# Kernel tuning notes

Hardware: AMD Instinct MI355X
Metric: run time of the kernel (lower is better)

## Reference

```python
import jax, jax.numpy as jnp
import numpy as np

N, C, D = 2048, 1000, 768
KNN = 5          # module default
SIGMA = 1.0      # unused by kNN affinity (matches original kNN_affinity)
BOUND_LAMBDA = 1.0
MAX_STEPS = 100


def setup_inputs() -> dict:
    key = jax.random.key(0)
    k1, k2 = jax.random.split(key)
    logits = jax.random.normal(k1, (N, C), dtype=jnp.float32) * 2.0
    feats = jax.random.normal(k2, (N, D), dtype=jnp.float32)
    return {"logits": logits, "feats": feats}


def _knn_affinity(feats, knn):
    # feats are L2-normalized, so squared euclidean dist = 2 - 2 * <xi, xj>
    n = feats.shape[0]
    sim = feats @ feats.T                                  # [N, N]
    dist = jnp.sqrt(jnp.clip(2.0 - 2.0 * sim, 0.0))        # [N, N]
    _, idx = jax.lax.top_k(-dist, knn + 1)                 # knn+1 smallest distances
    idx = idx[:, 1:]                                       # drop self (dist 0)
    W = jnp.zeros((n, n), dtype=feats.dtype)
    W = W.at[jnp.arange(n)[:, None], idx].set(1.0)
    return W


def _entropy_energy(Y, unary, pairwise, lam):
    return jnp.sum(unary * Y - lam * pairwise * Y + Y * jnp.log(jnp.clip(Y, 1e-20)))


def _laplacian_optimization(unary, kernel, lam=BOUND_LAMBDA, max_steps=MAX_STEPS):
    Y0 = jax.nn.softmax(-unary, axis=-1)

    def cond(state):
        _, _, i, done = state
        return (i < max_steps) & jnp.logical_not(done)

    def body(state):
        Y, oldE, i, _ = state
        pairwise = lam * (kernel @ Y)                      # [N, C]
        Ynew = jax.nn.softmax(pairwise - unary, axis=-1)
        E = _entropy_energy(Ynew, unary, pairwise, lam)
        done = (i > 1) & (jnp.abs(E - oldE) <= 1e-8 * jnp.abs(oldE))
        return (Ynew, E, i + 1, done)

    Y, _, _, _ = jax.lax.while_loop(
        cond, body, (Y0, jnp.float32(jnp.inf), jnp.int32(0), jnp.array(False))
    )
    return Y


def reference(logits, feats):
    probas = jax.nn.softmax(logits, axis=1)
    unary = -jnp.log(probas + 1e-10)                       # [N, C]
    f = feats / jnp.linalg.norm(feats, axis=-1, keepdims=True)
    kernel = _knn_affinity(f, KNN)                         # [N, N] binary
    kernel = 0.5 * (kernel + kernel.T)                     # force_symmetry=True
    return _laplacian_optimization(unary, kernel)
```

## Files before the change

kernel.cpp:

```cpp
#include <hip/hip_runtime.h>
#include <hip/hip_cooperative_groups.h>
#include <math.h>

namespace cg = cooperative_groups;

#define N_ 2048
#define C_ 1000
#define D_ 768
#define K_ 5
#define CAP_ 128
#define MAXS_ 100
#define LB_ 128
#define LT_ 512

typedef unsigned short ushort_t;
typedef unsigned int uint_t;

__device__ inline float bflo(uint_t v) { union { uint_t i; float f; } c; c.i = v << 16; return c.f; }
__device__ inline float bfhi(uint_t v) { union { uint_t i; float f; } c; c.i = v & 0xffff0000u; return c.f; }
__device__ inline ushort_t f2b(float f) {
    union { float f; uint_t i; } c; c.f = f;
    return (ushort_t)((c.i + 0x7fffu + ((c.i >> 16) & 1u)) >> 16);
}
__device__ inline uint_t pk(float a, float b) { return (uint_t)f2b(a) | ((uint_t)f2b(b) << 16); }

__global__ __launch_bounds__(256) void k_norm(const float* __restrict__ feats,
                                              float* __restrict__ fn) {
    const int r = blockIdx.x, tid = threadIdx.x;
    __shared__ float red[256];
    const float* row = feats + (size_t)r * D_;
    float ss = 0.f;
    for (int c = tid; c < D_; c += 256) { float v = row[c]; ss += v * v; }
    red[tid] = ss; __syncthreads();
    for (int s = 128; s > 0; s >>= 1) { if (tid < s) red[tid] += red[tid + s]; __syncthreads(); }
    const float n = sqrtf(red[0]); __syncthreads();
    for (int c = tid; c < D_; c += 256) fn[(size_t)r * D_ + c] = row[c] / n;
}

#define GTM 128
#define GTN 128
#define GBK 32
__global__ __launch_bounds__(512, 2) void k_gemm(const float* __restrict__ A,
                                                 float* __restrict__ Csim) {
    __shared__ float As[GBK][GTM + 4];
    __shared__ float Bs[GBK][GTN + 4];
    const int tid = threadIdx.x;
    const int tx = tid & 31;
    const int ty = tid >> 5;
    const int m0 = blockIdx.y * GTM, n0 = blockIdx.x * GTN;
    float acc[8][4] = {};
    for (int k0 = 0; k0 < D_; k0 += GBK) {
        #pragma unroll
        for (int l = 0; l < 2; l++) {
            int idx = tid + l * 512;
            int mm = idx >> 3, kk = (idx & 7) * 4;
            float4 v = *(const float4*)(A + (size_t)(m0 + mm) * D_ + k0 + kk);
            As[kk][mm] = v.x; As[kk + 1][mm] = v.y; As[kk + 2][mm] = v.z; As[kk + 3][mm] = v.w;
        }
        #pragma unroll
        for (int l = 0; l < 2; l++) {
            int idx = tid + l * 512;
            int mm = idx >> 3, kk = (idx & 7) * 4;
            float4 v = *(const float4*)(A + (size_t)(n0 + mm) * D_ + k0 + kk);
            Bs[kk][mm] = v.x; Bs[kk + 1][mm] = v.y; Bs[kk + 2][mm] = v.z; Bs[kk + 3][mm] = v.w;
        }
        __syncthreads();
        #pragma unroll
        for (int kk = 0; kk < GBK; kk++) {
            float4 a0 = *(const float4*)&As[kk][ty * 8];
            float4 a1 = *(const float4*)&As[kk][ty * 8 + 4];
            float4 bv = *(const float4*)&Bs[kk][tx * 4];
            float a[8] = { a0.x, a0.y, a0.z, a0.w, a1.x, a1.y, a1.z, a1.w };
            float b[4] = { bv.x, bv.y, bv.z, bv.w };
            #pragma unroll
            for (int i = 0; i < 8; i++)
                #pragma unroll
                for (int j = 0; j < 4; j++) acc[i][j] += a[i] * b[j];
        }
        __syncthreads();
    }
    #pragma unroll
    for (int i = 0; i < 8; i++) {
        float4 st = make_float4(acc[i][0], acc[i][1], acc[i][2], acc[i][3]);
        *(float4*)(Csim + (size_t)(m0 + ty * 8 + i) * N_ + n0 + tx * 4) = st;
    }
}

__global__ __launch_bounds__(256) void k_topk(const float* __restrict__ sim,
                                              int* __restrict__ knn) {
    const int r = blockIdx.x, tid = threadIdx.x;
    float bd[6]; int bi[6];
    #pragma unroll
    for (int k = 0; k < 6; k++) { bd[k] = INFINITY; bi[k] = 0x7fffffff; }
    const float* srow = sim + (size_t)r * N_;
    for (int j = tid; j < N_; j += 256) {
        float s = srow[j];
        float d = sqrtf(fmaxf(2.f - 2.f * s, 0.f));
        if (d < bd[5] || (d == bd[5] && j < bi[5])) {
            int k = 5;
            while (k > 0 && (d < bd[k - 1] || (d == bd[k - 1] && j < bi[k - 1]))) {
                bd[k] = bd[k - 1]; bi[k] = bi[k - 1]; k--;
            }
            bd[k] = d; bi[k] = j;
        }
    }
    __shared__ float sd[256][6];
    __shared__ int   si[256][6];
    #pragma unroll
    for (int k = 0; k < 6; k++) { sd[tid][k] = bd[k]; si[tid][k] = bi[k]; }
    __syncthreads();
    for (int s = 128; s > 0; s >>= 1) {
        if (tid < s) {
            float md[6]; int mi[6];
            int p = 0, q = 0;
            #pragma unroll
            for (int k = 0; k < 6; k++) {
                float d1 = sd[tid][p], d2 = sd[tid + s][q];
                int i1 = si[tid][p], i2 = si[tid + s][q];
                bool take1 = (d1 < d2) || (d1 == d2 && i1 < i2);
                if (take1) { md[k] = d1; mi[k] = i1; p++; } else { md[k] = d2; mi[k] = i2; q++; }
            }
            #pragma unroll
            for (int k = 0; k < 6; k++) { sd[tid][k] = md[k]; si[tid][k] = mi[k]; }
        }
        __syncthreads();
    }
    if (tid < K_) knn[(size_t)r * K_ + tid] = si[0][1 + tid];
}

__global__ __launch_bounds__(LT_) void k_lame(
    const float* __restrict__ logits, const int* __restrict__ knn,
    int* __restrict__ indeg, int* __restrict__ inlist,
    ushort_t* __restrict__ YA, ushort_t* __restrict__ YB,
    float* __restrict__ partials, int* __restrict__ flag,
    float* __restrict__ out)
{
    cg::grid_group grid = cg::this_grid();
    const int tid = threadIdx.x;
    const int wave = tid >> 6, lane = tid & 63;
    const int rbase = blockIdx.x * 16 + wave * 2;
    const int c0 = lane * 16;
    const bool msk0 = lane <= 62;
    const bool msk1 = lane <= 61;

    if (tid < 16) indeg[blockIdx.x * 16 + tid] = 0;
    grid.sync();
    if (tid < 16) {
        const int i = blockIdx.x * 16 + tid;
        #pragma unroll
        for (int k = 0; k < K_; k++) {
            const int j = knn[i * K_ + k];
            const int pos = atomicAdd(&indeg[j], 1);
            if (pos < CAP_) inlist[(size_t)j * CAP_ + pos] = i;
        }
    }
    grid.sync();

    __shared__ int nb[16][K_ + CAP_ + 3];
    __shared__ int cnts[16];
    #pragma unroll
    for (int rr = 0; rr < 2; rr++) {
        const int w = wave * 2 + rr, r = rbase + rr;
        if (lane == 0) cnts[w] = K_ + min(indeg[r], CAP_);
        if (lane < K_) nb[w][lane] = knn[r * K_ + lane];
        for (int t = lane; t < CAP_; t += 64) nb[w][K_ + t] = inlist[(size_t)r * CAP_ + t];
    }
    __syncthreads();
    if (lane < 2) {
        const int w = wave * 2 + lane;
        int* L = &nb[w][K_];
        const int cn = cnts[w] - K_;
        for (int a = 1; a < cn; a++) {
            const int key = L[a];
            int b = a - 1;
            while (b >= 0 && L[b] > key) { L[b + 1] = L[b]; b--; }
            L[b + 1] = key;
        }
    }
    __syncthreads();
    const int cnt2[2] = { cnts[wave * 2], cnts[wave * 2 + 1] };

    float u[2][16];
    #pragma unroll
    for (int rr = 0; rr < 2; rr++) {
        const float* lp = logits + (size_t)(rbase + rr) * C_;
        float l[16];
        #pragma unroll
        for (int q = 0; q < 4; q++) {
            const int off = c0 + q * 4;
            const int ao = (off + 3 < C_) ? off : 0;
            float4 v = *(const float4*)(lp + ao);
            l[q * 4 + 0] = v.x; l[q * 4 + 1] = v.y; l[q * 4 + 2] = v.z; l[q * 4 + 3] = v.w;
        }
        float mm = -INFINITY;
        #pragma unroll
        for (int k = 0; k < 8; k++) mm = fmaxf(mm, msk0 ? l[k] : -INFINITY);
        #pragma unroll
        for (int k = 8; k < 16; k++) mm = fmaxf(mm, msk1 ? l[k] : -INFINITY);
        #pragma unroll
        for (int o = 32; o > 0; o >>= 1) mm = fmaxf(mm, __shfl_xor(mm, o));
        float e[16];
        float s = 0.f;
        #pragma unroll
        for (int k = 0; k < 8; k++) { e[k] = msk0 ? expf(l[k] - mm) : 0.f; s += e[k]; }
        #pragma unroll
        for (int k = 8; k < 16; k++) { e[k] = msk1 ? expf(l[k] - mm) : 0.f; s += e[k]; }
        #pragma unroll
        for (int o = 32; o > 0; o >>= 1) s += __shfl_xor(s, o);
        const float inv = 1.f / s;
        #pragma unroll
        for (int k = 0; k < 16; k++) u[rr][k] = -logf(e[k] * inv + 1e-10f);
    }

    auto gather = [&](const ushort_t* __restrict__ src, int rr, float* acc) {
        const int w = wave * 2 + rr, cn = cnt2[rr];
        auto acc16 = [&](uint4 p, uint4 q) {
            acc[0] += bflo(p.x); acc[1] += bfhi(p.x); acc[2] += bflo(p.y); acc[3] += bfhi(p.y);
            acc[4] += bflo(p.z); acc[5] += bfhi(p.z); acc[6] += bflo(p.w); acc[7] += bfhi(p.w);
            acc[8] += bflo(q.x); acc[9] += bfhi(q.x); acc[10] += bflo(q.y); acc[11] += bfhi(q.y);
            acc[12] += bflo(q.z); acc[13] += bfhi(q.z); acc[14] += bflo(q.w); acc[15] += bfhi(q.w);
        };
        int t = 0;
        for (; t + 2 <= cn; t += 2) {
            const int n0 = nb[w][t], n1 = nb[w][t + 1];
            const uint4 p0 = *(const uint4*)(src + (size_t)n0 * C_ + c0);
            const uint4 p1 = *(const uint4*)(src + (size_t)n0 * C_ + c0 + 8);
            const uint4 q0 = *(const uint4*)(src + (size_t)n1 * C_ + c0);
            const uint4 q1 = *(const uint4*)(src + (size_t)n1 * C_ + c0 + 8);
            acc16(p0, p1); acc16(q0, q1);
        }
        if (t < cn) {
            const int n0 = nb[w][t];
            const uint4 p0 = *(const uint4*)(src + (size_t)n0 * C_ + c0);
            const uint4 p1 = *(const uint4*)(src + (size_t)n0 * C_ + c0 + 8);
            acc16(p0, p1);
        }
    };

    auto smax = [&](int rr, const float* acc, ushort_t* __restrict__ dst) -> float {
        const int r = rbase + rr;
        float z[16];
        #pragma unroll
        for (int k = 0; k < 16; k++) z[k] = 0.5f * acc[k] - u[rr][k];
        float mm = -INFINITY;
        #pragma unroll
        for (int k = 0; k < 8; k++) mm = fmaxf(mm, msk0 ? z[k] : -INFINITY);
        #pragma unroll
        for (int k = 8; k < 16; k++) mm = fmaxf(mm, msk1 ? z[k] : -INFINITY);
        #pragma unroll
        for (int o = 32; o > 0; o >>= 1) mm = fmaxf(mm, __shfl_xor(mm, o));
        float e[16];
        float s = 0.f;
        #pragma unroll
        for (int k = 0; k < 8; k++) { e[k] = msk0 ? expf(z[k] - mm) : 0.f; s += e[k]; }
        #pragma unroll
        for (int k = 8; k < 16; k++) { e[k] = msk1 ? expf(z[k] - mm) : 0.f; s += e[k]; }
        #pragma unroll
        for (int o = 32; o > 0; o >>= 1) s += __shfl_xor(s, o);
        const float inv = 1.f / s;
        if (msk0) {
            uint4 w;
            w.x = pk(e[0] * inv, e[1] * inv); w.y = pk(e[2] * inv, e[3] * inv);
            w.z = pk(e[4] * inv, e[5] * inv); w.w = pk(e[6] * inv, e[7] * inv);
            *(uint4*)(dst + (size_t)r * C_ + c0) = w;
        }
        if (msk1) {
            uint4 w;
            w.x = pk(e[8] * inv, e[9] * inv); w.y = pk(e[10] * inv, e[11] * inv);
            w.z = pk(e[12] * inv, e[13] * inv); w.w = pk(e[14] * inv, e[15] * inv);
            *(uint4*)(dst + (size_t)r * C_ + c0 + 8) = w;
        }
        return -(mm + logf(s));
    };

    {
        float zacc[16];
        #pragma unroll
        for (int k = 0; k < 16; k++) zacc[k] = 0.f;
        smax(0, zacc, YA);
        smax(1, zacc, YA);
    }
    if (blockIdx.x == 0 && tid == 0) { flag[0] = 0; flag[1] = 0; }
    grid.sync();

    float oldE = INFINITY;
    const ushort_t* fin = YB;
    for (int it = 0; it < MAXS_; ++it) {
        const ushort_t* src = (it & 1) ? YB : YA;
        ushort_t* dst = (it & 1) ? YA : YB;
        float acc0[16], acc1[16];
        #pragma unroll
        for (int k = 0; k < 16; k++) { acc0[k] = 0.f; acc1[k] = 0.f; }
        gather(src, 0, acc0);
        gather(src, 1, acc1);
        const float E0 = smax(0, acc0, dst);
        const float E1 = smax(1, acc1, dst);
        if (lane == 0) {
            partials[(size_t)(it & 1) * N_ + rbase] = E0;
            partials[(size_t)(it & 1) * N_ + rbase + 1] = E1;
        }
        grid.sync();
        if (blockIdx.x == 0 && wave == 0) {
            const float* P = partials + (size_t)(it & 1) * N_;
            float e = 0.f;
            #pragma unroll
            for (int q = 0; q < 32; q += 4) {
                float4 v = *(const float4*)(P + lane * 32 + q);
                e += ((v.x + v.y) + v.z) + v.w;
            }
            #pragma unroll
            for (int o = 32; o > 0; o >>= 1) e += __shfl_xor(e, o);
            const bool done = (it > 1) && (fabsf(e - oldE) <= 1e-8f * fabsf(oldE));
            oldE = e;
            if (lane == 0) flag[it & 1] = done ? 1 : 0;
        }
        fin = dst;
        if (((volatile const int*)flag)[(it + 1) & 1]) break;
    }

    #pragma unroll
    for (int rr = 0; rr < 2; rr++) {
        const int r = rbase + rr;
        #pragma unroll
        for (int q = 0; q < 4; q++) {
            if (c0 + q * 4 + 3 < C_) {
                const uint2 w = *(const uint2*)(fin + (size_t)r * C_ + c0 + q * 4);
                float4 o;
                o.x = bflo(w.x); o.y = bfhi(w.x); o.z = bflo(w.y); o.w = bfhi(w.y);
                *(float4*)(out + (size_t)r * C_ + c0 + q * 4) = o;
            }
        }
    }
}

extern "C" void kernel_launch(void* const* d_in, const int* in_sizes, int n_in,
                              void* d_out, int out_size, void* d_ws, size_t ws_size,
                              hipStream_t stream) {
    const float* logits = (const float*)d_in[0];
    const float* feats  = (const float*)d_in[1];
    float* out = (float*)d_out;
    char* ws = (char*)d_ws;

    size_t off = 0;
    auto alloc = [&](size_t b) { size_t o = off; off += (b + 255) & ~(size_t)255; return o; };
    float* fn      = (float*)(ws + alloc((size_t)N_ * D_ * 4));
    float* sim     = (float*)(ws + alloc((size_t)N_ * N_ * 4));
    int*   knn     = (int*)(ws + alloc((size_t)N_ * K_ * 4));
    int*   indeg   = (int*)(ws + alloc((size_t)N_ * 4));
    int*   inlist  = (int*)(ws + alloc((size_t)N_ * CAP_ * 4));
    float* partials= (float*)(ws + alloc((size_t)2 * N_ * 4));
    int*   flag    = (int*)(ws + alloc(256));
    if (off > ws_size) return;

    ushort_t* YA = (ushort_t*)sim;
    ushort_t* YB = YA + (size_t)N_ * C_;

    k_norm   <<<N_, 256, 0, stream>>>(feats, fn);
    k_gemm   <<<dim3(N_ / GTN, N_ / GTM), 512, 0, stream>>>(fn, sim);
    k_topk   <<<N_, 256, 0, stream>>>(sim, knn);

    const float* p_logits = logits;
    const int* p_knn = knn;
    int* p_indeg = indeg;
    int* p_inlist = inlist;
    ushort_t* p_YA = YA;
    ushort_t* p_YB = YB;
    float* p_part = partials;
    int* p_flag = flag;
    float* p_out = out;
    void* args[] = { &p_logits, &p_knn, &p_indeg, &p_inlist, &p_YA, &p_YB, &p_part, &p_flag, &p_out };
    (void)hipLaunchCooperativeKernel((void*)k_lame, dim3(LB_), dim3(LT_), args, 0, stream);
}
```

Baseline: 381.1 us.

## Fuse top-k selection into similarity GEMM epilogue and move graph build out

```diff
diff --git a/kernel.cpp b/kernel.cpp
--- a/kernel.cpp
+++ b/kernel.cpp
@@ -12,6 +12,7 @@
 #define MAXS_ 100
 #define LB_ 128
 #define LT_ 512
+#define NTILE_ 16
 
 typedef unsigned short ushort_t;
 typedef unsigned int uint_t;
@@ -41,7 +42,8 @@
 #define GTN 128
 #define GBK 32
 __global__ __launch_bounds__(512, 2) void k_gemm(const float* __restrict__ A,
-                                                 float* __restrict__ Csim) {
+                                                 float* __restrict__ cand_d,
+                                                 int* __restrict__ cand_j) {
     __shared__ float As[GBK][GTM + 4];
     __shared__ float Bs[GBK][GTN + 4];
     const int tid = threadIdx.x;
@@ -81,21 +83,62 @@
     }
     #pragma unroll
     for (int i = 0; i < 8; i++) {
-        float4 st = make_float4(acc[i][0], acc[i][1], acc[i][2], acc[i][3]);
-        *(float4*)(Csim + (size_t)(m0 + ty * 8 + i) * N_ + n0 + tx * 4) = st;
-    }
-}
-
-__global__ __launch_bounds__(256) void k_topk(const float* __restrict__ sim,
-                                              int* __restrict__ knn) {
-    const int r = blockIdx.x, tid = threadIdx.x;
+        float bd[6]; int bi[6];
+        #pragma unroll
+        for (int k = 0; k < 6; k++) { bd[k] = INFINITY; bi[k] = 0x7fffffff; }
+        #pragma unroll
+        for (int jj = 0; jj < 4; jj++) {
+            const float s = acc[i][jj];
+            const float d = sqrtf(fmaxf(2.f - 2.f * s, 0.f));
+            const int j = n0 + tx * 4 + jj;
+            if (d < bd[5] || (d == bd[5] && j < bi[5])) {
+                int k = 5;
+                while (k > 0 && (d < bd[k - 1] || (d == bd[k - 1] && j < bi[k - 1]))) {
+                    bd[k] = bd[k - 1]; bi[k] = bi[k - 1]; k--;
+                }
+                bd[k] = d; bi[k] = j;
+            }
+        }
+        #pragma unroll
+        for (int o = 1; o <= 16; o <<= 1) {
+            float od[6]; int oj[6];
+            #pragma unroll
+            for (int k = 0; k < 6; k++) { od[k] = __shfl_xor(bd[k], o); oj[k] = __shfl_xor(bi[k], o); }
+            float md[6]; int mi[6];
+            int p = 0, q = 0;
+            #pragma unroll
+            for (int k = 0; k < 6; k++) {
+                const bool take1 = (bd[p] < od[q]) || (bd[p] == od[q] && bi[p] < oj[q]);
+                if (take1) { md[k] = bd[p]; mi[k] = bi[p]; p++; }
+                else       { md[k] = od[q]; mi[k] = oj[q]; q++; }
+            }
+            #pragma unroll
+            for (int k = 0; k < 6; k++) { bd[k] = md[k]; bi[k] = mi[k]; }
+        }
+        if (tx == 0) {
+            const int r = m0 + ty * 8 + i;
+            const size_t base = ((size_t)r * NTILE_ + blockIdx.x) * 6;
+            #pragma unroll
+            for (int k = 0; k < 6; k++) { cand_d[base + k] = bd[k]; cand_j[base + k] = bi[k]; }
+        }
+    }
+}
+
+__global__ __launch_bounds__(256) void k_merge(const float* __restrict__ cand_d,
+                                               const int* __restrict__ cand_j,
+                                               int* __restrict__ knn,
+                                               int* __restrict__ indeg,
+                                               int* __restrict__ inlist) {
+    const int r = blockIdx.x * 256 + threadIdx.x;
+    if (r >= N_) return;
     float bd[6]; int bi[6];
     #pragma unroll
     for (int k = 0; k < 6; k++) { bd[k] = INFINITY; bi[k] = 0x7fffffff; }
-    const float* srow = sim + (size_t)r * N_;
-    for (int j = tid; j < N_; j += 256) {
-        float s = srow[j];
-        float d = sqrtf(fmaxf(2.f - 2.f * s, 0.f));
+    const float* cd = cand_d + (size_t)r * (NTILE_ * 6);
+    const int*   cj = cand_j + (size_t)r * (NTILE_ * 6);
+    for (int t = 0; t < NTILE_ * 6; t++) {
+        const float d = cd[t];
+        const int j = cj[t];
         if (d < bd[5] || (d == bd[5] && j < bi[5])) {
             int k = 5;
             while (k > 0 && (d < bd[k - 1] || (d == bd[k - 1] && j < bi[k - 1]))) {
@@ -104,33 +147,18 @@
             bd[k] = d; bi[k] = j;
         }
     }
-    __shared__ float sd[256][6];
-    __shared__ int   si[256][6];
-    #pragma unroll
-    for (int k = 0; k < 6; k++) { sd[tid][k] = bd[k]; si[tid][k] = bi[k]; }
-    __syncthreads();
-    for (int s = 128; s > 0; s >>= 1) {
-        if (tid < s) {
-            float md[6]; int mi[6];
-            int p = 0, q = 0;
-            #pragma unroll
-            for (int k = 0; k < 6; k++) {
-                float d1 = sd[tid][p], d2 = sd[tid + s][q];
-                int i1 = si[tid][p], i2 = si[tid + s][q];
-                bool take1 = (d1 < d2) || (d1 == d2 && i1 < i2);
-                if (take1) { md[k] = d1; mi[k] = i1; p++; } else { md[k] = d2; mi[k] = i2; q++; }
-            }
-            #pragma unroll
-            for (int k = 0; k < 6; k++) { sd[tid][k] = md[k]; si[tid][k] = mi[k]; }
-        }
-        __syncthreads();
-    }
-    if (tid < K_) knn[(size_t)r * K_ + tid] = si[0][1 + tid];
+    #pragma unroll
+    for (int k = 0; k < K_; k++) {
+        const int j = bi[1 + k];
+        knn[r * K_ + k] = j;
+        const int pos = atomicAdd(&indeg[j], 1);
+        if (pos < CAP_) inlist[(size_t)j * CAP_ + pos] = r;
+    }
 }
 
 __global__ __launch_bounds__(LT_) void k_lame(
     const float* __restrict__ logits, const int* __restrict__ knn,
-    int* __restrict__ indeg, int* __restrict__ inlist,
+    const int* __restrict__ indeg, const int* __restrict__ inlist,
     ushort_t* __restrict__ YA, ushort_t* __restrict__ YB,
     float* __restrict__ partials, int* __restrict__ flag,
     float* __restrict__ out)
@@ -142,19 +170,6 @@
     const int c0 = lane * 16;
     const bool msk0 = lane <= 62;
     const bool msk1 = lane <= 61;
-
-    if (tid < 16) indeg[blockIdx.x * 16 + tid] = 0;
-    grid.sync();
-    if (tid < 16) {
-        const int i = blockIdx.x * 16 + tid;
-        #pragma unroll
-        for (int k = 0; k < K_; k++) {
-            const int j = knn[i * K_ + k];
-            const int pos = atomicAdd(&indeg[j], 1);
-            if (pos < CAP_) inlist[(size_t)j * CAP_ + pos] = i;
-        }
-    }
-    grid.sync();
 
     __shared__ int nb[16][K_ + CAP_ + 3];
     __shared__ int cnts[16];
@@ -344,25 +359,28 @@
     size_t off = 0;
     auto alloc = [&](size_t b) { size_t o = off; off += (b + 255) & ~(size_t)255; return o; };
     float* fn      = (float*)(ws + alloc((size_t)N_ * D_ * 4));
-    float* sim     = (float*)(ws + alloc((size_t)N_ * N_ * 4));
+    float* ybuf    = (float*)(ws + alloc((size_t)2 * N_ * C_ * 2));
     int*   knn     = (int*)(ws + alloc((size_t)N_ * K_ * 4));
     int*   indeg   = (int*)(ws + alloc((size_t)N_ * 4));
     int*   inlist  = (int*)(ws + alloc((size_t)N_ * CAP_ * 4));
     float* partials= (float*)(ws + alloc((size_t)2 * N_ * 4));
     int*   flag    = (int*)(ws + alloc(256));
+    float* cand_d  = (float*)(ws + alloc((size_t)N_ * NTILE_ * 6 * 4));
+    int*   cand_j  = (int*)(ws + alloc((size_t)N_ * NTILE_ * 6 * 4));
     if (off > ws_size) return;
 
-    ushort_t* YA = (ushort_t*)sim;
+    ushort_t* YA = (ushort_t*)ybuf;
     ushort_t* YB = YA + (size_t)N_ * C_;
 
-    k_norm   <<<N_, 256, 0, stream>>>(feats, fn);
-    k_gemm   <<<dim3(N_ / GTN, N_ / GTM), 512, 0, stream>>>(fn, sim);
-    k_topk   <<<N_, 256, 0, stream>>>(sim, knn);
+    k_norm <<<N_, 256, 0, stream>>>(feats, fn);
+    (void)hipMemsetAsync(indeg, 0, (size_t)N_ * 4, stream);
+    k_gemm <<<dim3(N_ / GTN, N_ / GTM), 512, 0, stream>>>(fn, cand_d, cand_j);
+    k_merge<<<(N_ + 255) / 256, 256, 0, stream>>>(cand_d, cand_j, knn, indeg, inlist);
 
     const float* p_logits = logits;
     const int* p_knn = knn;
-    int* p_indeg = indeg;
-    int* p_inlist = inlist;
+    const int* p_indeg = indeg;
+    const int* p_inlist = inlist;
     ushort_t* p_YA = YA;
     ushort_t* p_YB = YB;
     float* p_part = partials;
```

After: 443.1 us. +16.3%, slower.
